# Performance work log

Hardware: AMD Instinct MI355X
Metric: run time of the kernel (lower is better)

The kernel has to match this reference:

```python
import jax, jax.numpy as jnp
import numpy as np

EMBED_DIM = 1024
HEAD_DIM = 64


def setup_inputs() -> dict:
    key = jax.random.key(0)
    ks = jax.random.split(key, 9)
    B, S, E, H = 4, 2048, EMBED_DIM, HEAD_DIM
    s = 1.0 / np.sqrt(E)
    return {
        "query": jax.random.normal(ks[0], (B, S, E), dtype=jnp.float32),
        "key": jax.random.normal(ks[1], (B, S, E), dtype=jnp.float32),
        "value": jax.random.normal(ks[2], (B, S, E), dtype=jnp.float32),
        "Wq": jax.random.normal(ks[3], (E, H), dtype=jnp.float32) * s,
        "bq": jnp.zeros((H,), dtype=jnp.float32),
        "Wk": jax.random.normal(ks[4], (E, H), dtype=jnp.float32) * s,
        "bk": jnp.zeros((H,), dtype=jnp.float32),
        "Wv": jax.random.normal(ks[5], (E, H), dtype=jnp.float32) * s,
        "bv": jnp.zeros((H,), dtype=jnp.float32),
    }


def reference(query, key, value, Wq, bq, Wk, bk, Wv, bv):
    # per-head linear projections: [B,S,E] @ [E,H] -> [B,S,H]
    q = jnp.einsum("bse,eh->bsh", query, Wq) + bq
    k = jnp.einsum("bse,eh->bsh", key, Wk) + bk
    v = jnp.einsum("bse,eh->bsh", value, Wv) + bv
    # NOTE: original code computes dim_k but never scales -> unscaled scores
    scores = jnp.einsum("bqh,bkh->bqk", q, k)  # [B,S,S]
    weights = jax.nn.softmax(scores, axis=-1)
    return jnp.einsum("bqk,bkh->bqh", weights, v)  # [B,S,H]
```

## Files before the change

### kernel.cpp

```cpp
#include <hip/hip_runtime.h>
#include <math.h>

#define B 4
#define S 2048
#define E 1024
#define H 64
#define BS (B*S)
#define LOG2E 1.44269504088896f
#define CINIT (-69.2493662f)

typedef float v4f __attribute__((ext_vector_type(4)));
typedef short v8s __attribute__((ext_vector_type(8)));
typedef unsigned short u16;
typedef u16 u16x8 __attribute__((ext_vector_type(8)));
typedef u16 u16x4 __attribute__((ext_vector_type(4)));

#define MFMA(a,b,c) __builtin_amdgcn_mfma_f32_16x16x32_bf16(a,b,c,0,0,0)

#define BARRIER_L() do { \
    asm volatile("s_waitcnt lgkmcnt(0)" ::: "memory"); \
    __builtin_amdgcn_s_barrier(); \
} while (0)

__device__ inline u16 rh_bf16(float x){ return (u16)((__float_as_uint(x)+0x8000u)>>16); }

__global__ __launch_bounds__(256) void wsetup_kernel(
    const float* __restrict__ Wq, const float* __restrict__ Wk,
    const float* __restrict__ Wv, u16* __restrict__ WF)
{
    __shared__ float wt[64][65];
    const int t  = threadIdx.x;
    const int p  = blockIdx.x >> 4;
    const int ec = blockIdx.x & 15, e0 = ec*64;
    const float* Wsrc = (p==0) ? Wq : (p==1 ? Wk : Wv);
    const float scale = (p==0) ? LOG2E : 1.0f;

    #pragma unroll
    for (int i=0;i<16;i++){
        int e_l = i*4 + (t>>6);
        wt[e_l][t&63] = Wsrc[(size_t)(e0+e_l)*H + (t&63)] * scale;
    }
    __syncthreads();

    u16* dst = WF + (((size_t)(p*16 + ec))*1024 + (size_t)t*4)*8;
    #pragma unroll
    for (int k=0;k<4;k++){
        const int c   = t*4 + k;
        const int l   = c & 63, b01 = (c>>6)&1, pl = (c>>7)&1, nt = c>>8;
        const int m   = l & 15, quad = l>>4;
        u16 o8[8];
        #pragma unroll
        for (int j=0;j<8;j++){
            float f = wt[b01*32 + quad*8 + j][nt*16 + m];
            unsigned u = __float_as_uint(f);
            if (pl==0) o8[j] = (u16)(u>>16);
            else       o8[j] = rh_bf16(f - __uint_as_float(u & 0xFFFF0000u));
        }
        *(u16x8*)(dst + (size_t)k*8) = *(u16x8*)&o8[0];
    }
}

__global__ __launch_bounds__(256) void proj_kernel(
    const float* __restrict__ query, const float* __restrict__ key_,
    const float* __restrict__ value,
    const u16* __restrict__ WF,
    const float* __restrict__ bq, const float* __restrict__ bk,
    const float* __restrict__ bv,
    u16* __restrict__ q_hi, u16* __restrict__ q_lo,
    u16* __restrict__ k_hi, u16* __restrict__ k_lo,
    u16* __restrict__ vt)
{
    __shared__ __align__(16) u16 vtile[64][40];

    const int t  = threadIdx.x;
    const int p  = blockIdx.x >> 8;
    const int r0 = (blockIdx.x & 255) * 32;
    const float* xp = (p==0) ? query : (p==1 ? key_ : value);
    const int wv = t>>6, lane = t&63, m = lane&15, quad = lane>>4;
    const int whalf = wv>>1, nh = wv&1;

    const float* xr = xp + (size_t)(r0 + whalf*16 + m)*E + quad*8;
    const u16* wfb = WF + (size_t)p*131072 + (size_t)nh*4096 + (size_t)lane*8;

    v4f acc0 = (v4f){0.f,0.f,0.f,0.f};
    v4f acc1 = (v4f){0.f,0.f,0.f,0.f};

#define LOADX(X, EC) {                                                         \
        const float* xa = xr + (size_t)(EC)*64;                                \
        X[0] = *(const float4*)(xa);                                           \
        X[1] = *(const float4*)(xa+4);                                         \
        X[2] = *(const float4*)(xa+32);                                        \
        X[3] = *(const float4*)(xa+36);                                        \
    }
#define LOADW(W, EC) {                                                         \
        const u16* wb = wfb + (size_t)(EC)*8192;                               \
        W[0] = *(const v8s*)(wb);                                              \
        W[1] = *(const v8s*)(wb+512);                                          \
        W[2] = *(const v8s*)(wb+1024);                                         \
        W[3] = *(const v8s*)(wb+1536);                                         \
        W[4] = *(const v8s*)(wb+2048);                                         \
        W[5] = *(const v8s*)(wb+2560);                                         \
        W[6] = *(const v8s*)(wb+3072);                                         \
        W[7] = *(const v8s*)(wb+3584);                                         \
    }
#define COMPUTE(X, W) {                                                        \
        float fv[16] = {X[0].x,X[0].y,X[0].z,X[0].w,                           \
                        X[1].x,X[1].y,X[1].z,X[1].w,                           \
                        X[2].x,X[2].y,X[2].z,X[2].w,                           \
                        X[3].x,X[3].y,X[3].z,X[3].w};                          \
        u16 ha[16], la[16];                                                    \
        _Pragma("unroll")                                                      \
        for (int j=0;j<16;j++){                                                \
            unsigned u = __float_as_uint(fv[j]);                               \
            ha[j] = (u16)(u>>16);                                              \
            la[j] = rh_bf16(fv[j] - __uint_as_float(u & 0xFFFF0000u));         \
        }                                                                      \
        v8s ah0 = *(v8s*)&ha[0], ah1 = *(v8s*)&ha[8];                          \
        v8s al0 = *(v8s*)&la[0], al1 = *(v8s*)&la[8];                          \
        v4f d0 = acc0;                                                         \
        d0 = MFMA(ah0,W[0],d0); d0 = MFMA(ah1,W[1],d0);                        \
        d0 = MFMA(al0,W[0],d0); d0 = MFMA(al1,W[1],d0);                        \
        d0 = MFMA(ah0,W[2],d0); d0 = MFMA(ah1,W[3],d0);                        \
        acc0 = d0;                                                             \
        v4f d1 = acc1;                                                         \
        d1 = MFMA(ah0,W[4],d1); d1 = MFMA(ah1,W[5],d1);                        \
        d1 = MFMA(al0,W[4],d1); d1 = MFMA(al1,W[5],d1);                        \
        d1 = MFMA(ah0,W[6],d1); d1 = MFMA(ah1,W[7],d1);                        \
        acc1 = d1;                                                             \
    }

    float4 xA[4], xB[4];
    v8s    wA[8], wB[8];
    LOADX(xA, 0); LOADW(wA, 0);
    LOADX(xB, 1); LOADW(wB, 1);

    #pragma unroll
    for (int ec2=0; ec2<16; ec2+=2){
        COMPUTE(xA, wA);
        if (ec2+2<16){ LOADX(xA, ec2+2); LOADW(wA, ec2+2); }
        COMPUTE(xB, wB);
        if (ec2+3<16){ LOADX(xB, ec2+3); LOADW(wB, ec2+3); }
    }
#undef LOADX
#undef LOADW
#undef COMPUTE

    const float* bp = (p==0) ? bq : (p==1 ? bk : bv);
    v4f accv[2]; accv[0] = acc0; accv[1] = acc1;
    if (p<2){
        const float bscale = (p==0) ? LOG2E : 1.0f;
        u16* dh = (p==0) ? q_hi : k_hi;
        u16* dl = (p==0) ? q_lo : k_lo;
        #pragma unroll
        for (int i=0;i<2;i++){
            const int hl = (nh*2+i)*16+m;
            const float bb = bp[hl]*bscale;
            #pragma unroll
            for (int r=0;r<4;r++){
                const int gr = r0 + whalf*16 + quad*4 + r;
                const float val = accv[i][r] + bb;
                unsigned u = __float_as_uint(val);
                u16 hi = (u16)(u>>16);
                float hif = __uint_as_float(u & 0xFFFF0000u);
                u16 lo = rh_bf16(val - hif);
                dh[(size_t)gr*H + hl] = hi;
                dl[(size_t)gr*H + hl] = lo;
            }
        }
    } else {
        const int rlb = whalf*16 + quad*4;
        #pragma unroll
        for (int i=0;i<2;i++){
            const int hl = (nh*2+i)*16+m;
            const float bb = bp[hl];
            u16 vv[4];
            #pragma unroll
            for (int r=0;r<4;r++) vv[r] = rh_bf16(accv[i][r] + bb);
            *(u16x4*)&vtile[hl][rlb] = *(u16x4*)&vv[0];
        }
        __syncthreads();
        const int h = t>>2, so = (t&3)*8;
        const int bidx = r0 >> 11, s0l = r0 & (S-1);
        u16* dst = vt + ((size_t)(bidx*H + h))*S + s0l + so;
        *(u16x8*)dst = *(const u16x8*)&vtile[h][so];
    }
}

__global__ __launch_bounds__(256) void attn_kernel(
    const u16* __restrict__ qh_g, const u16* __restrict__ ql_g,
    const u16* __restrict__ kh_g, const u16* __restrict__ kl_g,
    const u16* __restrict__ vt_g,
    float* __restrict__ accw, float* __restrict__ lw, int ksplit)
{
    __shared__ __align__(16) u16 khe[2][16][72];
    __shared__ __align__(16) u16 kle[2][16][72];
    __shared__ __align__(16) u16 vtl[64][40];
    __shared__ __align__(16) u16 pl[4][16][40];

    const int t = threadIdx.x;
    const int wv = t>>6, lane = t&63, m = lane&15, quad = lane>>4;
    const int bid = blockIdx.x;
    const int qb = bid / ksplit, chunk = bid % ksplit;
    const int b = qb >> 5, s0 = (qb & 31)*64;
    const int ck = S / ksplit;
    const int j0base = chunk * ck;
    const int iters = ck / 32;

    const u16* qr = qh_g + (size_t)(b*S + s0 + wv*16 + m)*H + quad*8;
    const u16* qrl = ql_g + (size_t)(b*S + s0 + wv*16 + m)*H + quad*8;
    const v8s qh0 = *(const v8s*)(qr),  qh1 = *(const v8s*)(qr+32);
    const v8s ql0 = *(const v8s*)(qrl), ql1 = *(const v8s*)(qrl+32);

    v4f oacc[4];
    #pragma unroll
    for (int nt=0;nt<4;nt++) oacc[nt] = (v4f){0.f,0.f,0.f,0.f};
    float lp[4] = {0.f,0.f,0.f,0.f};
    const v4f cinit = (v4f){CINIT,CINIT,CINIT,CINIT};

    const int sj = t>>3, sh8 = (t&7)*8;
    const u16* khs = kh_g + (size_t)(b*S + j0base + sj)*H + sh8;
    const u16* kls = kl_g + (size_t)(b*S + j0base + sj)*H + sh8;
    u16* khd = &khe[sj&1][sj>>1][sh8];
    u16* kld = &kle[sj&1][sj>>1][sh8];
    const int vh = t>>2, vj8 = (t&3)*8;
    const u16* vts = vt_g + (size_t)(b*H + vh)*S + j0base + vj8;
    u16* vtd = &vtl[vh][vj8];

    u16x8 khA, klA, vtA, khB, klB, vtB;
    khA = *(const u16x8*)khs;
    klA = *(const u16x8*)kls;
    vtA = *(const u16x8*)vts;
    khB = *(const u16x8*)(khs + (size_t)32*H);
    klB = *(const u16x8*)(kls + (size_t)32*H);
    vtB = *(const u16x8*)(vts + 32);

#define ATTN_ITER(IT, KHC, KLC, VTC, PREF)                                     \
    {                                                                          \
        BARRIER_L();                                                           \
        *(u16x8*)khd = KHC; *(u16x8*)kld = KLC; *(u16x8*)vtd = VTC;            \
        if (PREF){                                                             \
            KHC = *(const u16x8*)(khs + (size_t)((IT)+2)*32*H);                \
            KLC = *(const u16x8*)(kls + (size_t)((IT)+2)*32*H);                \
            VTC = *(const u16x8*)(vts + ((IT)+2)*32);                          \
        }                                                                      \
        BARRIER_L();                                                           \
                \
        v4f sc[2];                                                             \
        _Pragma("unroll")                                                      \
        for (int jt=0;jt<2;jt++){                                              \
            const u16* kr  = &khe[jt][m][quad*8];                              \
            const u16* krl = &kle[jt][m][quad*8];                              \
            v8s b0 = *(const v8s*)kr,  b1 = *(const v8s*)(kr+32);              \
            v8s c0 = *(const v8s*)krl, c1 = *(const v8s*)(krl+32);             \
            v4f d = cinit;                                                     \
            d = MFMA(qh0,b0,d); d = MFMA(qh1,b1,d);                            \
            d = MFMA(ql0,b0,d); d = MFMA(ql1,b1,d);                            \
            d = MFMA(qh0,c0,d); d = MFMA(qh1,c1,d);                            \
            sc[jt] = d;                                                        \
        }                                                                      \
            \
        _Pragma("unroll")                                                      \
        for (int r=0;r<4;r++){                                                 \
            float p0 = exp2f(sc[0][r]);                     \
            float p1 = exp2f(sc[1][r]);                     \
            lp[r] += p0 + p1;                                                  \
            unsigned pk = ((__float_as_uint(p0)+0x8000u)>>16)                  \
                        | ((__float_as_uint(p1)+0x8000u) & 0xFFFF0000u);       \
            *(unsigned*)&pl[wv][quad*4+r][2*m] = pk;                           \
        }                                                                      \
          \
        v8s pa = *(const v8s*)&pl[wv][m][quad*8];                              \
        _Pragma("unroll")                                                      \
        for (int nt=0;nt<4;nt++){                                              \
            v8s vb = *(const v8s*)&vtl[nt*16+m][quad*8];                       \
            oacc[nt] = MFMA(pa, vb, oacc[nt]);                                 \
        }                                                                      \
    }

    for (int it=0; it<iters; it+=2){
        ATTN_ITER(it,   khA,klA,vtA, (it+2<iters))
        ATTN_ITER(it+1, khB,klB,vtB, (it+3<iters))
    }
#undef ATTN_ITER

    #pragma unroll
    for (int r=0;r<4;r++){
        float v = lp[r];
        v += __shfl_xor(v,1); v += __shfl_xor(v,2);
        v += __shfl_xor(v,4); v += __shfl_xor(v,8);
        lp[r] = v;
    }
    const int growb = b*S + s0 + wv*16;
    if (m==0){
        float4 lv; lv.x=lp[0]; lv.y=lp[1]; lv.z=lp[2]; lv.w=lp[3];
        *(float4*)(lw + (size_t)chunk*BS + growb + quad*4) = lv;
    }
    float* ab = accw + ((size_t)chunk*BS + growb)*H;
    #pragma unroll
    for (int nt=0;nt<4;nt++){
        #pragma unroll
        for (int r=0;r<4;r++)
            ab[(size_t)(quad*4+r)*H + nt*16 + m] = oacc[nt][r];
    }
}

__global__ __launch_bounds__(256) void merge_kernel(
    const float* __restrict__ accw, const float* __restrict__ lw,
    float* __restrict__ out, int ksplit)
{
    const int idx = blockIdx.x*256 + threadIdx.x;
    const int row = idx >> 4, h4 = (idx & 15)*4;
    float4 a = {0.f,0.f,0.f,0.f};
    float ls = 0.f;
    for (int c=0;c<ksplit;c++){
        const float4 t4 = *(const float4*)(accw + ((size_t)c*BS + row)*H + h4);
        a.x+=t4.x; a.y+=t4.y; a.z+=t4.z; a.w+=t4.w;
        ls += lw[(size_t)c*BS + row];
    }
    const float inv = __builtin_amdgcn_rcpf(ls);
    float4 o; o.x=a.x*inv; o.y=a.y*inv; o.z=a.z*inv; o.w=a.w*inv;
    *(float4*)(out + (size_t)row*H + h4) = o;
}

extern "C" void kernel_launch(void* const* d_in, const int* in_sizes, int n_in,
                              void* d_out, int out_size, void* d_ws, size_t ws_size,
                              hipStream_t stream) {
    const float* query = (const float*)d_in[0];
    const float* key_  = (const float*)d_in[1];
    const float* value = (const float*)d_in[2];
    const float* Wq    = (const float*)d_in[3];
    const float* bq    = (const float*)d_in[4];
    const float* Wk    = (const float*)d_in[5];
    const float* bk    = (const float*)d_in[6];
    const float* Wv    = (const float*)d_in[7];
    const float* bv    = (const float*)d_in[8];
    float* out = (float*)d_out;

    char* base = (char*)d_ws;
    size_t off = 0;
    u16* WF    = (u16*)(base + off); off += (size_t)3*16*1024*8*2;
    u16* q_hi  = (u16*)(base + off); off += (size_t)BS*H*2;
    u16* q_lo  = (u16*)(base + off); off += (size_t)BS*H*2;
    u16* k_hi  = (u16*)(base + off); off += (size_t)BS*H*2;
    u16* k_lo  = (u16*)(base + off); off += (size_t)BS*H*2;
    u16* vt    = (u16*)(base + off); off += (size_t)BS*H*2;
    const size_t fixed = off;
    const size_t CH = (size_t)BS*H*4 + (size_t)BS*4;

    int K = 1;
    if      (ws_size >= fixed + 8*CH) K = 8;
    else if (ws_size >= fixed + 4*CH) K = 4;
    else if (ws_size >= fixed + 2*CH) K = 2;

    float* lw   = (float*)(base + fixed);
    float* accw = (float*)(base + fixed + (size_t)K*BS*4);

    wsetup_kernel<<<48, 256, 0, stream>>>(Wq, Wk, Wv, WF);
    proj_kernel<<<768, 256, 0, stream>>>(query, key_, value, WF,
                                         bq, bk, bv, q_hi, q_lo, k_hi, k_lo, vt);
    attn_kernel<<<128*K, 256, 0, stream>>>(q_hi, q_lo, k_hi, k_lo, vt, accw, lw, K);
    merge_kernel<<<512, 256, 0, stream>>>(accw, lw, out, K);
}
```

Before: 183.3 us.

## Stage projection inputs and weights through LDS via async global-to-LDS loads

```diff
diff --git a/kernel.cpp b/kernel.cpp
--- a/kernel.cpp
+++ b/kernel.cpp
@@ -12,6 +12,7 @@
 typedef float v4f __attribute__((ext_vector_type(4)));
 typedef short v8s __attribute__((ext_vector_type(8)));
 typedef unsigned short u16;
+typedef unsigned int u32;
 typedef u16 u16x8 __attribute__((ext_vector_type(8)));
 typedef u16 u16x4 __attribute__((ext_vector_type(4)));
 
@@ -22,16 +23,23 @@
     __builtin_amdgcn_s_barrier(); \
 } while (0)
 
+__device__ __forceinline__ void gl_lds16(const void* g, void* l){
+    __builtin_amdgcn_global_load_lds(
+        (const __attribute__((address_space(1))) u32*)g,
+        (__attribute__((address_space(3))) u32*)l, 16, 0, 0);
+}
+
 __device__ inline u16 rh_bf16(float x){ return (u16)((__float_as_uint(x)+0x8000u)>>16); }
 
 __global__ __launch_bounds__(256) void wsetup_kernel(
     const float* __restrict__ Wq, const float* __restrict__ Wk,
-    const float* __restrict__ Wv, u16* __restrict__ WF)
+    const float* __restrict__ Wv,
+    u16* __restrict__ Wt_hi, u16* __restrict__ Wt_lo)
 {
     __shared__ float wt[64][65];
     const int t  = threadIdx.x;
     const int p  = blockIdx.x >> 4;
-    const int ec = blockIdx.x & 15, e0 = ec*64;
+    const int e0 = (blockIdx.x & 15) * 64;
     const float* Wsrc = (p==0) ? Wq : (p==1 ? Wk : Wv);
     const float scale = (p==0) ? LOG2E : 1.0f;
 
@@ -42,35 +50,38 @@
     }
     __syncthreads();
 
-    u16* dst = WF + (((size_t)(p*16 + ec))*1024 + (size_t)t*4)*8;
-    #pragma unroll
-    for (int k=0;k<4;k++){
-        const int c   = t*4 + k;
-        const int l   = c & 63, b01 = (c>>6)&1, pl = (c>>7)&1, nt = c>>8;
-        const int m   = l & 15, quad = l>>4;
-        u16 o8[8];
-        #pragma unroll
-        for (int j=0;j<8;j++){
-            float f = wt[b01*32 + quad*8 + j][nt*16 + m];
-            unsigned u = __float_as_uint(f);
-            if (pl==0) o8[j] = (u16)(u>>16);
-            else       o8[j] = rh_bf16(f - __uint_as_float(u & 0xFFFF0000u));
-        }
-        *(u16x8*)(dst + (size_t)k*8) = *(u16x8*)&o8[0];
-    }
+    const int h = t>>2, e16 = (t&3)*16;
+    u16 hi_a[16], lo_a[16];
+    #pragma unroll
+    for (int j=0;j<16;j++){
+        float f = wt[e16+j][h];
+        unsigned u = __float_as_uint(f);
+        hi_a[j] = (u16)(u>>16);
+        float hif = __uint_as_float(u & 0xFFFF0000u);
+        lo_a[j] = rh_bf16(f - hif);
+    }
+    u16* dh = Wt_hi + (size_t)(p*64+h)*E + e0 + e16;
+    u16* dl = Wt_lo + (size_t)(p*64+h)*E + e0 + e16;
+    *(u16x8*)dh     = *(u16x8*)&hi_a[0];
+    *(u16x8*)(dh+8) = *(u16x8*)&hi_a[8];
+    *(u16x8*)dl     = *(u16x8*)&lo_a[0];
+    *(u16x8*)(dl+8) = *(u16x8*)&lo_a[8];
 }
 
 __global__ __launch_bounds__(256) void proj_kernel(
     const float* __restrict__ query, const float* __restrict__ key_,
     const float* __restrict__ value,
-    const u16* __restrict__ WF,
+    const u16* __restrict__ Wt_hi, const u16* __restrict__ Wt_lo,
     const float* __restrict__ bq, const float* __restrict__ bk,
     const float* __restrict__ bv,
     u16* __restrict__ q_hi, u16* __restrict__ q_lo,
     u16* __restrict__ k_hi, u16* __restrict__ k_lo,
     u16* __restrict__ vt)
 {
-    __shared__ __align__(16) u16 vtile[64][40];
+    __shared__ __align__(16) float xs[2][32][64];
+    __shared__ __align__(16) u16  wsh[2][64][64];
+    __shared__ __align__(16) u16  wsl[2][64][64];
+    __shared__ __align__(16) u16  vtile[64][40];
 
     const int t  = threadIdx.x;
     const int p  = blockIdx.x >> 8;
@@ -79,70 +90,81 @@
     const int wv = t>>6, lane = t&63, m = lane&15, quad = lane>>4;
     const int whalf = wv>>1, nh = wv&1;
 
-    const float* xr = xp + (size_t)(r0 + whalf*16 + m)*E + quad*8;
-    const u16* wfb = WF + (size_t)p*131072 + (size_t)nh*4096 + (size_t)lane*8;
+    const int xr0_ = t>>4,        xc0_ = t&15;
+    const int xr1_ = (256+t)>>4,  xc1_ = (256+t)&15;
+    const float* xg0 = xp + (size_t)(r0+xr0_)*E + (size_t)(xc0_ ^ (xr0_&15))*4;
+    const float* xg1 = xp + (size_t)(r0+xr1_)*E + (size_t)(xc1_ ^ (xr1_&15))*4;
+    const int wr0_ = t>>3,        wc0_ = t&7;
+    const int wr1_ = (256+t)>>3,  wc1_ = (256+t)&7;
+    const u16* whg0 = Wt_hi + (size_t)(p*64+wr0_)*E + (size_t)(wc0_ ^ (wr0_&7))*8;
+    const u16* whg1 = Wt_hi + (size_t)(p*64+wr1_)*E + (size_t)(wc1_ ^ (wr1_&7))*8;
+    const u16* wlg0 = Wt_lo + (size_t)(p*64+wr0_)*E + (size_t)(wc0_ ^ (wr0_&7))*8;
+    const u16* wlg1 = Wt_lo + (size_t)(p*64+wr1_)*E + (size_t)(wc1_ ^ (wr1_&7))*8;
 
     v4f acc0 = (v4f){0.f,0.f,0.f,0.f};
     v4f acc1 = (v4f){0.f,0.f,0.f,0.f};
 
-#define LOADX(X, EC) {                                                         \
-        const float* xa = xr + (size_t)(EC)*64;                                \
-        X[0] = *(const float4*)(xa);                                           \
-        X[1] = *(const float4*)(xa+4);                                         \
-        X[2] = *(const float4*)(xa+32);                                        \
-        X[3] = *(const float4*)(xa+36);                                        \
-    }
-#define LOADW(W, EC) {                                                         \
-        const u16* wb = wfb + (size_t)(EC)*8192;                               \
-        W[0] = *(const v8s*)(wb);                                              \
-        W[1] = *(const v8s*)(wb+512);                                          \
-        W[2] = *(const v8s*)(wb+1024);                                         \
-        W[3] = *(const v8s*)(wb+1536);                                         \
-        W[4] = *(const v8s*)(wb+2048);                                         \
-        W[5] = *(const v8s*)(wb+2560);                                         \
-        W[6] = *(const v8s*)(wb+3072);                                         \
-        W[7] = *(const v8s*)(wb+3584);                                         \
-    }
-#define COMPUTE(X, W) {                                                        \
-        float fv[16] = {X[0].x,X[0].y,X[0].z,X[0].w,                           \
-                        X[1].x,X[1].y,X[1].z,X[1].w,                           \
-                        X[2].x,X[2].y,X[2].z,X[2].w,                           \
-                        X[3].x,X[3].y,X[3].z,X[3].w};                          \
+#define STAGE(BUF, EC) {                                                       \
+        const float* xo0 = xg0 + (size_t)(EC)*64;                              \
+        const float* xo1 = xg1 + (size_t)(EC)*64;                              \
+        gl_lds16(xo0, &xs[BUF][0][0] + (size_t)t*4);                           \
+        gl_lds16(xo1, &xs[BUF][0][0] + (size_t)(256+t)*4);                     \
+        const size_t wo = (size_t)(EC)*64;                                     \
+        gl_lds16(whg0 + wo, &wsh[BUF][0][0] + (size_t)t*8);                    \
+        gl_lds16(whg1 + wo, &wsh[BUF][0][0] + (size_t)(256+t)*8);              \
+        gl_lds16(wlg0 + wo, &wsl[BUF][0][0] + (size_t)t*8);                    \
+        gl_lds16(wlg1 + wo, &wsl[BUF][0][0] + (size_t)(256+t)*8);              \
+    }
+
+#define COMPUTE(BUF) {                                                         \
+        const int arow = whalf*16 + m;                                         \
+        const int rx = arow & 15;                                              \
+        float fA[16];                                                          \
+        *(float4*)&fA[0]  = *(const float4*)&xs[BUF][arow][((quad*2  )^rx)*4]; \
+        *(float4*)&fA[4]  = *(const float4*)&xs[BUF][arow][((quad*2+1)^rx)*4]; \
+        *(float4*)&fA[8]  = *(const float4*)&xs[BUF][arow][((8+quad*2)^rx)*4]; \
+        *(float4*)&fA[12] = *(const float4*)&xs[BUF][arow][((9+quad*2)^rx)*4]; \
         u16 ha[16], la[16];                                                    \
         _Pragma("unroll")                                                      \
         for (int j=0;j<16;j++){                                                \
-            unsigned u = __float_as_uint(fv[j]);                               \
+            unsigned u = __float_as_uint(fA[j]);                               \
             ha[j] = (u16)(u>>16);                                              \
-            la[j] = rh_bf16(fv[j] - __uint_as_float(u & 0xFFFF0000u));         \
+            la[j] = rh_bf16(fA[j] - __uint_as_float(u & 0xFFFF0000u));         \
         }                                                                      \
         v8s ah0 = *(v8s*)&ha[0], ah1 = *(v8s*)&ha[8];                          \
         v8s al0 = *(v8s*)&la[0], al1 = *(v8s*)&la[8];                          \
+        const int wrow0 = (nh*2+0)*16 + m, wx0 = wrow0 & 7;                    \
+        const int wrow1 = (nh*2+1)*16 + m, wx1 = wrow1 & 7;                    \
+        v8s bh00 = *(const v8s*)&wsh[BUF][wrow0][((quad  )^wx0)*8];            \
+        v8s bh01 = *(const v8s*)&wsh[BUF][wrow0][((4+quad)^wx0)*8];            \
+        v8s bl00 = *(const v8s*)&wsl[BUF][wrow0][((quad  )^wx0)*8];            \
+        v8s bl01 = *(const v8s*)&wsl[BUF][wrow0][((4+quad)^wx0)*8];            \
+        v8s bh10 = *(const v8s*)&wsh[BUF][wrow1][((quad  )^wx1)*8];            \
+        v8s bh11 = *(const v8s*)&wsh[BUF][wrow1][((4+quad)^wx1)*8];            \
+        v8s bl10 = *(const v8s*)&wsl[BUF][wrow1][((quad  )^wx1)*8];            \
+        v8s bl11 = *(const v8s*)&wsl[BUF][wrow1][((4+quad)^wx1)*8];            \
         v4f d0 = acc0;                                                         \
-        d0 = MFMA(ah0,W[0],d0); d0 = MFMA(ah1,W[1],d0);                        \
-        d0 = MFMA(al0,W[0],d0); d0 = MFMA(al1,W[1],d0);                        \
-        d0 = MFMA(ah0,W[2],d0); d0 = MFMA(ah1,W[3],d0);                        \
+        d0 = MFMA(ah0,bh00,d0); d0 = MFMA(ah1,bh01,d0);                        \
+        d0 = MFMA(al0,bh00,d0); d0 = MFMA(al1,bh01,d0);                        \
+        d0 = MFMA(ah0,bl00,d0); d0 = MFMA(ah1,bl01,d0);                        \
         acc0 = d0;                                                             \
         v4f d1 = acc1;                                                         \
-        d1 = MFMA(ah0,W[4],d1); d1 = MFMA(ah1,W[5],d1);                        \
-        d1 = MFMA(al0,W[4],d1); d1 = MFMA(al1,W[5],d1);                        \
-        d1 = MFMA(ah0,W[6],d1); d1 = MFMA(ah1,W[7],d1);                        \
+        d1 = MFMA(ah0,bh10,d1); d1 = MFMA(ah1,bh11,d1);                        \
+        d1 = MFMA(al0,bh10,d1); d1 = MFMA(al1,bh11,d1);                        \
+        d1 = MFMA(ah0,bl10,d1); d1 = MFMA(ah1,bl11,d1);                        \
         acc1 = d1;                                                             \
     }
 
-    float4 xA[4], xB[4];
-    v8s    wA[8], wB[8];
-    LOADX(xA, 0); LOADW(wA, 0);
-    LOADX(xB, 1); LOADW(wB, 1);
-
-    #pragma unroll
-    for (int ec2=0; ec2<16; ec2+=2){
-        COMPUTE(xA, wA);
-        if (ec2+2<16){ LOADX(xA, ec2+2); LOADW(wA, ec2+2); }
-        COMPUTE(xB, wB);
-        if (ec2+3<16){ LOADX(xB, ec2+3); LOADW(wB, ec2+3); }
-    }
-#undef LOADX
-#undef LOADW
+    STAGE(0, 0);
+    __syncthreads();
+    #pragma unroll
+    for (int ec=0; ec<16; ++ec){
+        const int CUR = ec & 1;
+        if (ec+1 < 16) STAGE(CUR^1, ec+1);
+        COMPUTE(CUR);
+        __syncthreads();
+    }
+#undef STAGE
 #undef COMPUTE
 
     const float* bp = (p==0) ? bq : (p==1 ? bk : bv);
@@ -338,7 +360,8 @@
 
     char* base = (char*)d_ws;
     size_t off = 0;
-    u16* WF    = (u16*)(base + off); off += (size_t)3*16*1024*8*2;
+    u16* Wt_hi = (u16*)(base + off); off += (size_t)3*64*E*2;
+    u16* Wt_lo = (u16*)(base + off); off += (size_t)3*64*E*2;
     u16* q_hi  = (u16*)(base + off); off += (size_t)BS*H*2;
     u16* q_lo  = (u16*)(base + off); off += (size_t)BS*H*2;
     u16* k_hi  = (u16*)(base + off); off += (size_t)BS*H*2;
@@ -355,8 +378,8 @@
     float* lw   = (float*)(base + fixed);
     float* accw = (float*)(base + fixed + (size_t)K*BS*4);
 
-    wsetup_kernel<<<48, 256, 0, stream>>>(Wq, Wk, Wv, WF);
-    proj_kernel<<<768, 256, 0, stream>>>(query, key_, value, WF,
+    wsetup_kernel<<<48, 256, 0, stream>>>(Wq, Wk, Wv, Wt_hi, Wt_lo);
+    proj_kernel<<<768, 256, 0, stream>>>(query, key_, value, Wt_hi, Wt_lo,
                                          bq, bk, bv, q_hi, q_lo, k_hi, k_lo, vt);
     attn_kernel<<<128*K, 256, 0, stream>>>(q_hi, q_lo, k_hi, k_lo, vt, accw, lw, K);
     merge_kernel<<<512, 256, 0, stream>>>(accw, lw, out, K);
```

Result: no change. 183.8 us (+0.3%).

## Share split-bf16 X conversion through LDS in projection and retune attention prefetch

Applied to the files above, without the earlier changes.

```diff
diff --git a/kernel.cpp b/kernel.cpp
--- a/kernel.cpp
+++ b/kernel.cpp
@@ -60,7 +60,7 @@
     }
 }
 
-__global__ __launch_bounds__(256) void proj_kernel(
+__global__ __launch_bounds__(128, 3) void proj_kernel(
     const float* __restrict__ query, const float* __restrict__ key_,
     const float* __restrict__ value,
     const u16* __restrict__ WF,
@@ -70,95 +70,96 @@
     u16* __restrict__ k_hi, u16* __restrict__ k_lo,
     u16* __restrict__ vt)
 {
-    __shared__ __align__(16) u16 vtile[64][40];
+    __shared__ __align__(16) u16 xh[16][72], xl[16][72];
+    __shared__ __align__(16) u16 vtile[64][24];
 
     const int t  = threadIdx.x;
-    const int p  = blockIdx.x >> 8;
-    const int r0 = (blockIdx.x & 255) * 32;
+    const int p  = blockIdx.x >> 9;
+    const int r0 = (blockIdx.x & 511) * 16;
     const float* xp = (p==0) ? query : (p==1 ? key_ : value);
     const int wv = t>>6, lane = t&63, m = lane&15, quad = lane>>4;
-    const int whalf = wv>>1, nh = wv&1;
-
-    const float* xr = xp + (size_t)(r0 + whalf*16 + m)*E + quad*8;
-    const u16* wfb = WF + (size_t)p*131072 + (size_t)nh*4096 + (size_t)lane*8;
-
-    v4f acc0 = (v4f){0.f,0.f,0.f,0.f};
-    v4f acc1 = (v4f){0.f,0.f,0.f,0.f};
+
+    const int sxr = t>>3, sxc = (t&7)*8;
+    const float* xb = xp + (size_t)(r0+sxr)*E + sxc;
+
+    const u16* wfb = WF + (size_t)p*131072 + (size_t)wv*4096 + (size_t)lane*8;
+
+    v4f acc[2];
+    acc[0] = (v4f){0.f,0.f,0.f,0.f};
+    acc[1] = (v4f){0.f,0.f,0.f,0.f};
+
+    float4 xA[2], xB[2];
+    v8s    wA[8], wB[8];
 
 #define LOADX(X, EC) {                                                         \
-        const float* xa = xr + (size_t)(EC)*64;                                \
+        const float* xa = xb + (EC)*64;                                        \
         X[0] = *(const float4*)(xa);                                           \
         X[1] = *(const float4*)(xa+4);                                         \
-        X[2] = *(const float4*)(xa+32);                                        \
-        X[3] = *(const float4*)(xa+36);                                        \
     }
 #define LOADW(W, EC) {                                                         \
         const u16* wb = wfb + (size_t)(EC)*8192;                               \
-        W[0] = *(const v8s*)(wb);                                              \
-        W[1] = *(const v8s*)(wb+512);                                          \
-        W[2] = *(const v8s*)(wb+1024);                                         \
-        W[3] = *(const v8s*)(wb+1536);                                         \
-        W[4] = *(const v8s*)(wb+2048);                                         \
-        W[5] = *(const v8s*)(wb+2560);                                         \
-        W[6] = *(const v8s*)(wb+3072);                                         \
-        W[7] = *(const v8s*)(wb+3584);                                         \
-    }
-#define COMPUTE(X, W) {                                                        \
-        float fv[16] = {X[0].x,X[0].y,X[0].z,X[0].w,                           \
-                        X[1].x,X[1].y,X[1].z,X[1].w,                           \
-                        X[2].x,X[2].y,X[2].z,X[2].w,                           \
-                        X[3].x,X[3].y,X[3].z,X[3].w};                          \
-        u16 ha[16], la[16];                                                    \
-        _Pragma("unroll")                                                      \
-        for (int j=0;j<16;j++){                                                \
-            unsigned u = __float_as_uint(fv[j]);                               \
-            ha[j] = (u16)(u>>16);                                              \
-            la[j] = rh_bf16(fv[j] - __uint_as_float(u & 0xFFFF0000u));         \
-        }                                                                      \
-        v8s ah0 = *(v8s*)&ha[0], ah1 = *(v8s*)&ha[8];                          \
-        v8s al0 = *(v8s*)&la[0], al1 = *(v8s*)&la[8];                          \
-        v4f d0 = acc0;                                                         \
-        d0 = MFMA(ah0,W[0],d0); d0 = MFMA(ah1,W[1],d0);                        \
-        d0 = MFMA(al0,W[0],d0); d0 = MFMA(al1,W[1],d0);                        \
-        d0 = MFMA(ah0,W[2],d0); d0 = MFMA(ah1,W[3],d0);                        \
-        acc0 = d0;                                                             \
-        v4f d1 = acc1;                                                         \
-        d1 = MFMA(ah0,W[4],d1); d1 = MFMA(ah1,W[5],d1);                        \
-        d1 = MFMA(al0,W[4],d1); d1 = MFMA(al1,W[5],d1);                        \
-        d1 = MFMA(ah0,W[6],d1); d1 = MFMA(ah1,W[7],d1);                        \
-        acc1 = d1;                                                             \
-    }
-
-    float4 xA[4], xB[4];
-    v8s    wA[8], wB[8];
+        W[0] = *(const v8s*)(wb);          W[1] = *(const v8s*)(wb+512);       \
+        W[2] = *(const v8s*)(wb+1024);     W[3] = *(const v8s*)(wb+1536);      \
+        W[4] = *(const v8s*)(wb+2048);     W[5] = *(const v8s*)(wb+2560);      \
+        W[6] = *(const v8s*)(wb+3072);     W[7] = *(const v8s*)(wb+3584);      \
+    }
+#define PHASE(EC, XC, WC, PREF)                                                \
+    {                                                                          \
+        BARRIER_L();                         \
+        {                                                                      \
+            float fv[8] = {XC[0].x,XC[0].y,XC[0].z,XC[0].w,                    \
+                           XC[1].x,XC[1].y,XC[1].z,XC[1].w};                   \
+            u16 ha[8], la[8];                                                  \
+            _Pragma("unroll")                                                  \
+            for (int j=0;j<8;j++){                                             \
+                unsigned u = __float_as_uint(fv[j]);                           \
+                ha[j] = (u16)(u>>16);                                          \
+                la[j] = rh_bf16(fv[j] - __uint_as_float(u & 0xFFFF0000u));     \
+            }                                                                  \
+            *(u16x8*)&xh[sxr][sxc] = *(u16x8*)&ha[0];                          \
+            *(u16x8*)&xl[sxr][sxc] = *(u16x8*)&la[0];                          \
+        }                                                                      \
+        BARRIER_L();                                       \
+        v8s ah0 = *(const v8s*)&xh[m][quad*8];                                 \
+        v8s ah1 = *(const v8s*)&xh[m][32+quad*8];                              \
+        v8s al0 = *(const v8s*)&xl[m][quad*8];                                 \
+        v8s al1 = *(const v8s*)&xl[m][32+quad*8];                              \
+        v4f d0 = acc[0];                                                       \
+        d0 = MFMA(ah0,WC[0],d0); d0 = MFMA(ah1,WC[1],d0);                      \
+        d0 = MFMA(al0,WC[0],d0); d0 = MFMA(al1,WC[1],d0);                      \
+        d0 = MFMA(ah0,WC[2],d0); d0 = MFMA(ah1,WC[3],d0);                      \
+        acc[0] = d0;                                                           \
+        v4f d1 = acc[1];                                                       \
+        d1 = MFMA(ah0,WC[4],d1); d1 = MFMA(ah1,WC[5],d1);                      \
+        d1 = MFMA(al0,WC[4],d1); d1 = MFMA(al1,WC[5],d1);                      \
+        d1 = MFMA(ah0,WC[6],d1); d1 = MFMA(ah1,WC[7],d1);                      \
+        acc[1] = d1;                                                           \
+        if (PREF){ LOADX(XC, (EC)+2); LOADW(WC, (EC)+2); }                     \
+    }
+
     LOADX(xA, 0); LOADW(wA, 0);
     LOADX(xB, 1); LOADW(wB, 1);
-
-    #pragma unroll
     for (int ec2=0; ec2<16; ec2+=2){
-        COMPUTE(xA, wA);
-        if (ec2+2<16){ LOADX(xA, ec2+2); LOADW(wA, ec2+2); }
-        COMPUTE(xB, wB);
-        if (ec2+3<16){ LOADX(xB, ec2+3); LOADW(wB, ec2+3); }
+        PHASE(ec2,   xA, wA, (ec2+2<16))
+        PHASE(ec2+1, xB, wB, (ec2+3<16))
     }
 #undef LOADX
 #undef LOADW
-#undef COMPUTE
+#undef PHASE
 
     const float* bp = (p==0) ? bq : (p==1 ? bk : bv);
-    v4f accv[2]; accv[0] = acc0; accv[1] = acc1;
     if (p<2){
         const float bscale = (p==0) ? LOG2E : 1.0f;
         u16* dh = (p==0) ? q_hi : k_hi;
         u16* dl = (p==0) ? q_lo : k_lo;
         #pragma unroll
         for (int i=0;i<2;i++){
-            const int hl = (nh*2+i)*16+m;
+            const int hl = wv*32 + i*16 + m;
             const float bb = bp[hl]*bscale;
             #pragma unroll
             for (int r=0;r<4;r++){
-                const int gr = r0 + whalf*16 + quad*4 + r;
-                const float val = accv[i][r] + bb;
+                const int gr = r0 + quad*4 + r;
+                const float val = acc[i][r] + bb;
                 unsigned u = __float_as_uint(val);
                 u16 hi = (u16)(u>>16);
                 float hif = __uint_as_float(u & 0xFFFF0000u);
@@ -168,25 +169,24 @@
             }
         }
     } else {
-        const int rlb = whalf*16 + quad*4;
         #pragma unroll
         for (int i=0;i<2;i++){
-            const int hl = (nh*2+i)*16+m;
+            const int hl = wv*32 + i*16 + m;
             const float bb = bp[hl];
             u16 vv[4];
             #pragma unroll
-            for (int r=0;r<4;r++) vv[r] = rh_bf16(accv[i][r] + bb);
-            *(u16x4*)&vtile[hl][rlb] = *(u16x4*)&vv[0];
+            for (int r=0;r<4;r++) vv[r] = rh_bf16(acc[i][r] + bb);
+            *(u16x4*)&vtile[hl][quad*4] = *(u16x4*)&vv[0];
         }
         __syncthreads();
-        const int h = t>>2, so = (t&3)*8;
+        const int h = t>>1, so = (t&1)*8;
         const int bidx = r0 >> 11, s0l = r0 & (S-1);
         u16* dst = vt + ((size_t)(bidx*H + h))*S + s0l + so;
         *(u16x8*)dst = *(const u16x8*)&vtile[h][so];
     }
 }
 
-__global__ __launch_bounds__(256) void attn_kernel(
+__global__ __launch_bounds__(256, 4) void attn_kernel(
     const u16* __restrict__ qh_g, const u16* __restrict__ ql_g,
     const u16* __restrict__ kh_g, const u16* __restrict__ kl_g,
     const u16* __restrict__ vt_g,
@@ -230,20 +230,17 @@
     khA = *(const u16x8*)khs;
     klA = *(const u16x8*)kls;
     vtA = *(const u16x8*)vts;
-    khB = *(const u16x8*)(khs + (size_t)32*H);
-    klB = *(const u16x8*)(kls + (size_t)32*H);
-    vtB = *(const u16x8*)(vts + 32);
-
-#define ATTN_ITER(IT, KHC, KLC, VTC, PREF)                                     \
+
+#define ATTN_ITER(IT, KHC, KLC, VTC, KHN, KLN, VTN, PREF)                      \
     {                                                                          \
-        BARRIER_L();                                                           \
+        __syncthreads();                                                       \
         *(u16x8*)khd = KHC; *(u16x8*)kld = KLC; *(u16x8*)vtd = VTC;            \
         if (PREF){                                                             \
-            KHC = *(const u16x8*)(khs + (size_t)((IT)+2)*32*H);                \
-            KLC = *(const u16x8*)(kls + (size_t)((IT)+2)*32*H);                \
-            VTC = *(const u16x8*)(vts + ((IT)+2)*32);                          \
-        }                                                                      \
-        BARRIER_L();                                                           \
+            KHN = *(const u16x8*)(khs + (size_t)((IT)+1)*32*H);                \
+            KLN = *(const u16x8*)(kls + (size_t)((IT)+1)*32*H);                \
+            VTN = *(const u16x8*)(vts + ((IT)+1)*32);                          \
+        }                                                                      \
+        __syncthreads();                                                       \
                 \
         v4f sc[2];                                                             \
         _Pragma("unroll")                                                      \
@@ -278,8 +275,8 @@
     }
 
     for (int it=0; it<iters; it+=2){
-        ATTN_ITER(it,   khA,klA,vtA, (it+2<iters))
-        ATTN_ITER(it+1, khB,klB,vtB, (it+3<iters))
+        ATTN_ITER(it,   khA,klA,vtA, khB,klB,vtB, true)
+        ATTN_ITER(it+1, khB,klB,vtB, khA,klA,vtA, (it+2<iters))
     }
 #undef ATTN_ITER
 
@@ -356,8 +353,8 @@
     float* accw = (float*)(base + fixed + (size_t)K*BS*4);
 
     wsetup_kernel<<<48, 256, 0, stream>>>(Wq, Wk, Wv, WF);
-    proj_kernel<<<768, 256, 0, stream>>>(query, key_, value, WF,
-                                         bq, bk, bv, q_hi, q_lo, k_hi, k_lo, vt);
+    proj_kernel<<<1536, 128, 0, stream>>>(query, key_, value, WF,
+                                          bq, bk, bv, q_hi, q_lo, k_hi, k_lo, vt);
     attn_kernel<<<128*K, 256, 0, stream>>>(q_hi, q_lo, k_hi, k_lo, vt, accw, lw, K);
     merge_kernel<<<512, 256, 0, stream>>>(accw, lw, out, K);
 }
```

After: 176.3 us. -3.8%, faster.
